# Kernel optimization log

Measured on AMD Instinct MI355X. Metric: run time of the kernel, lower is better.

Reference implementation:

```python
import jax, jax.numpy as jnp
import numpy as np


def setup_inputs() -> dict:
    key = jax.random.key(0)
    k1, k2 = jax.random.split(key)
    b, n, d = 4, 4096, 1024
    x = jax.random.normal(k1, (b, n, d), dtype=jnp.float32)
    t = jax.random.normal(k2, (2 * n, d), dtype=jnp.float32)
    return {"x": x, "t": t}


def reference(x, t):
    # x: (b, n, d); t: (2*l, d) with l = max(n, m); m = n here.
    n = x.shape[1]
    m = n
    l = max(n, m)
    L = 2 * l
    x_fft = jnp.fft.rfft(x, n=L, axis=-2)            # (b, L//2+1, d) complex
    t_fft = jnp.fft.rfft(t[None, :, :], n=L, axis=-2)  # (1, L//2+1, d)
    o = jnp.fft.irfft(x_fft * t_fft, n=L, axis=-2)   # (b, L, d)
    return o[:, :m]
```

## Files before the change

### kernel.cpp

```cpp
#include <hip/hip_runtime.h>
#include <hip/hip_bf16.h>

#define NFFT 8192
#define NH   4096
#define D    1024
#define NSEQ 4096
#define NDP  512
#define BATCH 4
#define NT   512
#define TSLOT 4097
#define PI_D 3.14159265358979323846

#define C1 0.92387953251128675613f
#define S1 0.38268343236508977173f
#define RT 0.70710678118654752440f

__device__ __forceinline__ int SWZ(int i) { return i ^ ((i >> 4) & 15) ^ ((i >> 8) & 15); }

__device__ __forceinline__ float2 cadd(float2 a, float2 b){ return make_float2(a.x+b.x, a.y+b.y); }
__device__ __forceinline__ float2 csub(float2 a, float2 b){ return make_float2(a.x-b.x, a.y-b.y); }
__device__ __forceinline__ float2 cmul(float2 a, float2 w){ return make_float2(a.x*w.x - a.y*w.y, a.x*w.y + a.y*w.x); }
__device__ __forceinline__ float2 cmulc(float2 a, float2 w){ return make_float2(a.x*w.x + a.y*w.y, a.y*w.x - a.x*w.y); }

__device__ __forceinline__ int drev16(int k) {
    return ((k & 1) << 12) | (((k >> 1) & 15) << 8) | (((k >> 5) & 15) << 4) | ((k >> 9) & 15);
}
__device__ __forceinline__ int kmap16(int tid, int it) {
    return ((tid >> 7) & 3) | (it << 2) | ((tid & 15) << 5) | (((tid >> 4) & 7) << 9);
}

__global__ __launch_bounds__(256) void wtab_init(float2* __restrict__ wtab) {
    int m = blockIdx.x * 256 + threadIdx.x;
    double a = -2.0 * PI_D * (double)m / (double)NFFT;
    wtab[m] = make_float2((float)cos(a), (float)sin(a));
}

template<int H, bool TW, bool INV>
__device__ __forceinline__ void pass16(float2* zs, const float2* __restrict__ wt, int t) {
    int blk = t >> 8;
    int i0, tw1i;
    if (H == 256)      { int j = t & 255;                      i0 = blk*4096 + j;           tw1i = 2*j;  }
    else if (H == 16)  { int g = (t>>4) & 15; int j = t & 15;  i0 = blk*4096 + g*256 + j;   tw1i = 32*j; }
    else               { int g = t & 255;                      i0 = blk*4096 + g*16;        tw1i = 0;    }

    float2 w1, w2, w3, w4, w8, w12;
    if (TW) {
        w1 = wt[tw1i];
        w2 = cmul(w1, w1);  w3 = cmul(w2, w1);
        w4 = cmul(w2, w2);  w8 = cmul(w4, w4);  w12 = cmul(w8, w4);
    }

    float2 v[16];
    #pragma unroll
    for (int q = 0; q < 16; ++q) v[q] = zs[SWZ(i0 + H*q)];

    if (INV && TW) {
        v[1]=cmulc(v[1],w1);  v[2]=cmulc(v[2],w2);  v[3]=cmulc(v[3],w3);
        v[4]=cmulc(v[4],w4);  v[5]=cmulc(v[5],cmul(w4,w1));  v[6]=cmulc(v[6],cmul(w4,w2));  v[7]=cmulc(v[7],cmul(w4,w3));
        v[8]=cmulc(v[8],w8);  v[9]=cmulc(v[9],cmul(w8,w1));  v[10]=cmulc(v[10],cmul(w8,w2)); v[11]=cmulc(v[11],cmul(w8,w3));
        v[12]=cmulc(v[12],w12); v[13]=cmulc(v[13],cmul(w12,w1)); v[14]=cmulc(v[14],cmul(w12,w2)); v[15]=cmulc(v[15],cmul(w12,w3));
    }

    float2 s[4][4];
    #pragma unroll
    for (int i = 0; i < 4; ++i) {
        float2 z0=v[i], z1=v[i+4], z2=v[i+8], z3=v[i+12];
        float2 A=cadd(z0,z2), Cc=csub(z0,z2), B=cadd(z1,z3), Dd=csub(z1,z3);
        s[i][0] = cadd(A,B);
        s[i][2] = csub(A,B);
        if (!INV) { s[i][1] = make_float2(Cc.x+Dd.y, Cc.y-Dd.x);
                    s[i][3] = make_float2(Cc.x-Dd.y, Cc.y+Dd.x); }
        else      { s[i][1] = make_float2(Cc.x-Dd.y, Cc.y+Dd.x);
                    s[i][3] = make_float2(Cc.x+Dd.y, Cc.y-Dd.x); }
    }
    if (!INV) {
        s[1][1]=cmul(s[1][1],make_float2(C1,-S1)); s[1][2]=cmul(s[1][2],make_float2(RT,-RT)); s[1][3]=cmul(s[1][3],make_float2(S1,-C1));
        s[2][1]=cmul(s[2][1],make_float2(RT,-RT)); s[2][2]=make_float2(s[2][2].y,-s[2][2].x); s[2][3]=cmul(s[2][3],make_float2(-RT,-RT));
        s[3][1]=cmul(s[3][1],make_float2(S1,-C1)); s[3][2]=cmul(s[3][2],make_float2(-RT,-RT)); s[3][3]=cmul(s[3][3],make_float2(-C1,S1));
    } else {
        s[1][1]=cmul(s[1][1],make_float2(C1,S1));  s[1][2]=cmul(s[1][2],make_float2(RT,RT));  s[1][3]=cmul(s[1][3],make_float2(S1,C1));
        s[2][1]=cmul(s[2][1],make_float2(RT,RT));  s[2][2]=make_float2(-s[2][2].y,s[2][2].x); s[2][3]=cmul(s[2][3],make_float2(-RT,RT));
        s[3][1]=cmul(s[3][1],make_float2(S1,C1));  s[3][2]=cmul(s[3][2],make_float2(-RT,RT)); s[3][3]=cmul(s[3][3],make_float2(-C1,-S1));
    }
    float2 y[16];
    #pragma unroll
    for (int o = 0; o < 4; ++o) {
        float2 z0=s[0][o], z1=s[1][o], z2=s[2][o], z3=s[3][o];
        float2 A=cadd(z0,z2), Cc=csub(z0,z2), B=cadd(z1,z3), Dd=csub(z1,z3);
        y[o]    = cadd(A,B);
        y[o+8]  = csub(A,B);
        if (!INV) { y[o+4]  = make_float2(Cc.x+Dd.y, Cc.y-Dd.x);
                    y[o+12] = make_float2(Cc.x-Dd.y, Cc.y+Dd.x); }
        else      { y[o+4]  = make_float2(Cc.x-Dd.y, Cc.y+Dd.x);
                    y[o+12] = make_float2(Cc.x+Dd.y, Cc.y-Dd.x); }
    }

    if (!INV && TW) {
        y[1]=cmul(y[1],w1);  y[2]=cmul(y[2],w2);  y[3]=cmul(y[3],w3);
        y[4]=cmul(y[4],w4);  y[5]=cmul(y[5],cmul(w4,w1));  y[6]=cmul(y[6],cmul(w4,w2));  y[7]=cmul(y[7],cmul(w4,w3));
        y[8]=cmul(y[8],w8);  y[9]=cmul(y[9],cmul(w8,w1));  y[10]=cmul(y[10],cmul(w8,w2)); y[11]=cmul(y[11],cmul(w8,w3));
        y[12]=cmul(y[12],w12); y[13]=cmul(y[13],cmul(w12,w1)); y[14]=cmul(y[14],cmul(w12,w2)); y[15]=cmul(y[15],cmul(w12,w3));
    }
    #pragma unroll
    for (int r = 0; r < 16; ++r) zs[SWZ(i0 + H*r)] = y[r];
}

template<int PACKED>
__global__ __launch_bounds__(NT, 2) void tspec_kernel(const float2* __restrict__ tP,
                                                      const float* __restrict__ tg,
                                                      const float2* __restrict__ wt,
                                                      float4* __restrict__ tspecU) {
    __shared__ float2 zs[NFFT];
    int t  = threadIdx.x;
    int dp = blockIdx.x;

    if (PACKED) {
        const float2* slab = tP + (size_t)dp * NFFT;
        #pragma unroll
        for (int it = 0; it < 8; ++it) {
            int idx = t + it * NT;
            float2 v0 = slab[idx], v1 = slab[idx + NH];
            zs[SWZ(idx)]      = cadd(v0, v1);
            zs[SWZ(idx + NH)] = cmul(csub(v0, v1), wt[idx]);
        }
    } else {
        const float* tb = tg + 2 * dp;
        #pragma unroll
        for (int it = 0; it < 8; ++it) {
            int idx = t + it * NT;
            float2 v0 = *(const float2*)(tb + (size_t)idx * D);
            float2 v1 = *(const float2*)(tb + (size_t)(idx + NH) * D);
            zs[SWZ(idx)]      = cadd(v0, v1);
            zs[SWZ(idx + NH)] = cmul(csub(v0, v1), wt[idx]);
        }
    }
    __syncthreads();
    pass16<256, true,  false>(zs, wt, t); __syncthreads();
    pass16<16,  true,  false>(zs, wt, t); __syncthreads();
    pass16<1,   false, false>(zs, wt, t); __syncthreads();

    float4* o = tspecU + (size_t)dp * TSLOT;
    #pragma unroll
    for (int it = 0; it < 8; ++it) {
        int k  = kmap16(t, it);
        int p1 = drev16(k);
        int p2 = drev16((NFFT - k) & (NFFT - 1));
        float2 z1 = zs[SWZ(p1)], z2 = zs[SWZ(p2)];
        o[it * NT + t] = make_float4(0.5f*(z1.x + z2.x), 0.5f*(z1.y - z2.y),
                                     0.5f*(z1.y + z2.y), 0.5f*(z2.x - z1.x));
    }
    if (t == 0) {
        float2 zn = zs[SWZ(8)];
        o[4096] = make_float4(zn.x, 0.f, zn.y, 0.f);
    }
}

template<int PACKED>
__global__ __launch_bounds__(NT, 2) void conv_kernel(float2* __restrict__ xP,
                                                     const float* __restrict__ xg,
                                                     float* __restrict__ outg,
                                                     const float2* __restrict__ wt,
                                                     const float4* __restrict__ tspecU) {
    __shared__ float2 zs[NFFT];
    int t  = threadIdx.x;
    int dp = blockIdx.x;
    int b  = blockIdx.y;

    float2* slab = PACKED ? (xP + ((size_t)dp * BATCH + b) * NSEQ) : nullptr;
    if (PACKED) {
        #pragma unroll
        for (int it = 0; it < 8; ++it) {
            int idx = t + it * NT;
            float2 v = slab[idx];
            zs[SWZ(idx)]      = v;
            zs[SWZ(idx + NH)] = cmul(v, wt[idx]);
        }
    } else {
        const float* xb = xg + (size_t)b * NSEQ * D + 2 * dp;
        #pragma unroll
        for (int it = 0; it < 8; ++it) {
            int idx = t + it * NT;
            float2 v = *(const float2*)(xb + (size_t)idx * D);
            zs[SWZ(idx)]      = v;
            zs[SWZ(idx + NH)] = cmul(v, wt[idx]);
        }
    }
    __syncthreads();
    pass16<256, true,  false>(zs, wt, t); __syncthreads();
    pass16<16,  true,  false>(zs, wt, t); __syncthreads();
    pass16<1,   false, false>(zs, wt, t); __syncthreads();

    const float4* ts4 = tspecU + (size_t)dp * TSLOT;
    #pragma unroll
    for (int it = 0; it < 8; ++it) {
        int k  = kmap16(t, it);
        int p1 = drev16(k);
        int p2 = drev16((NFFT - k) & (NFFT - 1));
        float2 z1 = zs[SWZ(p1)], z2 = zs[SWZ(p2)];
        float4 T  = ts4[it * NT + t];
        float x0r = 0.5f*(z1.x + z2.x), x0i = 0.5f*(z1.y - z2.y);
        float x1r = 0.5f*(z1.y + z2.y), x1i = 0.5f*(z2.x - z1.x);
        float y0r = x0r*T.x - x0i*T.y, y0i = x0r*T.y + x0i*T.x;
        float y1r = x1r*T.z - x1i*T.w, y1i = x1r*T.w + x1i*T.z;
        zs[SWZ(p1)] = make_float2(y0r - y1i, y0i + y1r);
        zs[SWZ(p2)] = make_float2(y0r + y1i, y1r - y0i);
    }
    if (t == 0) {
        float4 T = ts4[4096];
        float2 zn = zs[SWZ(8)];
        zs[SWZ(8)] = make_float2(zn.x * T.x, zn.y * T.z);
    }
    __syncthreads();

    pass16<1,   false, true>(zs, wt, t); __syncthreads();
    pass16<16,  true,  true>(zs, wt, t); __syncthreads();
    pass16<256, true,  true>(zs, wt, t); __syncthreads();

    const float sc = 1.0f / (float)NFFT;
    if (PACKED) {
        #pragma unroll
        for (int it = 0; it < 8; ++it) {
            int n = t + it * NT;
            float2 a  = zs[SWZ(n)];
            float2 bb = zs[SWZ(n + NH)];
            float2 r  = cadd(a, cmulc(bb, wt[n]));
            slab[n] = make_float2(r.x * sc, r.y * sc);
        }
    } else {
        float* ob = outg + (size_t)b * NSEQ * D + 2 * dp;
        #pragma unroll
        for (int it = 0; it < 8; ++it) {
            int n = t + it * NT;
            float2 a  = zs[SWZ(n)];
            float2 bb = zs[SWZ(n + NH)];
            float2 r  = cadd(a, cmulc(bb, wt[n]));
            *(float2*)(ob + (size_t)n * D) = make_float2(r.x * sc, r.y * sc);
        }
    }
}

__global__ __launch_bounds__(256) void pack_kernel(const float* __restrict__ in,
                                                   float2* __restrict__ outp,
                                                   int Nrows, int Bsz) {
    __shared__ float tile[64][65];
    int tid = threadIdx.x;
    int n0 = blockIdx.x * 64;
    int d0 = blockIdx.y * 64;
    int b  = blockIdx.z;
    const float* ib = in + (size_t)b * Nrows * D;
    #pragma unroll
    for (int it = 0; it < 16; ++it) {
        int n_l = it * 4 + (tid >> 6);
        int d_l = tid & 63;
        tile[n_l][d_l] = ib[(size_t)(n0 + n_l) * D + d0 + d_l];
    }
    __syncthreads();
    #pragma unroll
    for (int it = 0; it < 8; ++it) {
        int flat = it * 256 + tid;
        int dp_l = flat >> 6;
        int n_l  = flat & 63;
        float2 v = make_float2(tile[n_l][2*dp_l], tile[n_l][2*dp_l + 1]);
        outp[((size_t)(d0/2 + dp_l) * Bsz + b) * (size_t)Nrows + n0 + n_l] = v;
    }
}

__global__ __launch_bounds__(256) void unpack_kernel(const float2* __restrict__ in,
                                                     float* __restrict__ outp) {
    __shared__ float tile[64][65];
    int tid = threadIdx.x;
    int n0 = blockIdx.x * 64;
    int d0 = blockIdx.y * 64;
    int b  = blockIdx.z;
    #pragma unroll
    for (int it = 0; it < 8; ++it) {
        int flat = it * 256 + tid;
        int dp_l = flat >> 6;
        int n_l  = flat & 63;
        float2 v = in[((size_t)(d0/2 + dp_l) * BATCH + b) * (size_t)NSEQ + n0 + n_l];
        tile[n_l][2*dp_l]     = v.x;
        tile[n_l][2*dp_l + 1] = v.y;
    }
    __syncthreads();
    float* ob = outp + (size_t)b * NSEQ * D;
    #pragma unroll
    for (int it = 0; it < 16; ++it) {
        int n_l = it * 4 + (tid >> 6);
        int d_l = tid & 63;
        ob[(size_t)(n0 + n_l) * D + d0 + d_l] = tile[n_l][d_l];
    }
}

extern "C" void kernel_launch(void* const* d_in, const int* in_sizes, int n_in,
                              void* d_out, int out_size, void* d_ws, size_t ws_size,
                              hipStream_t stream) {
    const float* x = (const float*)d_in[0];
    const float* t = (const float*)d_in[1];
    float* outp = (float*)d_out;

    char* ws = (char*)d_ws;
    float2* wtab   = (float2*)ws;
    float4* tspecU = (float4*)(ws + 65536);
    const size_t OFF_REGION = 65536 + (size_t)NDP * TSLOT * 16;
    float2* region = (float2*)(ws + OFF_REGION);
    const size_t need_full = OFF_REGION + (size_t)NDP * BATCH * NSEQ * sizeof(float2);

    wtab_init<<<16, 256, 0, stream>>>(wtab);

    if (ws_size >= need_full) {
        pack_kernel<<<dim3(128, 16, 1), 256, 0, stream>>>(t, region, NFFT, 1);
        tspec_kernel<1><<<NDP, NT, 0, stream>>>(region, nullptr, wtab, tspecU);
        pack_kernel<<<dim3(64, 16, BATCH), 256, 0, stream>>>(x, region, NSEQ, BATCH);
        conv_kernel<1><<<dim3(NDP, BATCH, 1), NT, 0, stream>>>(region, nullptr, nullptr, wtab, tspecU);
        unpack_kernel<<<dim3(64, 16, BATCH), 256, 0, stream>>>(region, outp);
    } else {
        tspec_kernel<0><<<NDP, NT, 0, stream>>>(nullptr, t, wtab, tspecU);
        conv_kernel<0><<<dim3(NDP, BATCH, 1), NT, 0, stream>>>(nullptr, x, outp, wtab, tspecU);
    }
}
```

Baseline: 188.0 us.

## Fuse first/last FFT passes with global load/store and spectrum pointwise in registers

The first radix-16 pass now runs directly on values loaded from global memory, and the last inverse pass feeds the output store, so the separate LDS staging round trips are gone. The final forward pass and the pointwise spectrum multiply plus the first inverse pass stay in registers. Each thread reads its conjugate-pair partner from a computed mirror chunk instead of bit-reversed scattered reads. This removes several shared-memory passes and barriers. In exchange it adds complex index logic and keeps more registers live, which may reduce occupancy.

```diff
diff --git a/kernel.cpp b/kernel.cpp
--- a/kernel.cpp
+++ b/kernel.cpp
@@ -22,45 +22,14 @@
 __device__ __forceinline__ float2 cmul(float2 a, float2 w){ return make_float2(a.x*w.x - a.y*w.y, a.x*w.y + a.y*w.x); }
 __device__ __forceinline__ float2 cmulc(float2 a, float2 w){ return make_float2(a.x*w.x + a.y*w.y, a.y*w.x - a.x*w.y); }
 
-__device__ __forceinline__ int drev16(int k) {
-    return ((k & 1) << 12) | (((k >> 1) & 15) << 8) | (((k >> 5) & 15) << 4) | ((k >> 9) & 15);
-}
-__device__ __forceinline__ int kmap16(int tid, int it) {
-    return ((tid >> 7) & 3) | (it << 2) | ((tid & 15) << 5) | (((tid >> 4) & 7) << 9);
-}
-
 __global__ __launch_bounds__(256) void wtab_init(float2* __restrict__ wtab) {
     int m = blockIdx.x * 256 + threadIdx.x;
     double a = -2.0 * PI_D * (double)m / (double)NFFT;
     wtab[m] = make_float2((float)cos(a), (float)sin(a));
 }
 
-template<int H, bool TW, bool INV>
-__device__ __forceinline__ void pass16(float2* zs, const float2* __restrict__ wt, int t) {
-    int blk = t >> 8;
-    int i0, tw1i;
-    if (H == 256)      { int j = t & 255;                      i0 = blk*4096 + j;           tw1i = 2*j;  }
-    else if (H == 16)  { int g = (t>>4) & 15; int j = t & 15;  i0 = blk*4096 + g*256 + j;   tw1i = 32*j; }
-    else               { int g = t & 255;                      i0 = blk*4096 + g*16;        tw1i = 0;    }
-
-    float2 w1, w2, w3, w4, w8, w12;
-    if (TW) {
-        w1 = wt[tw1i];
-        w2 = cmul(w1, w1);  w3 = cmul(w2, w1);
-        w4 = cmul(w2, w2);  w8 = cmul(w4, w4);  w12 = cmul(w8, w4);
-    }
-
-    float2 v[16];
-    #pragma unroll
-    for (int q = 0; q < 16; ++q) v[q] = zs[SWZ(i0 + H*q)];
-
-    if (INV && TW) {
-        v[1]=cmulc(v[1],w1);  v[2]=cmulc(v[2],w2);  v[3]=cmulc(v[3],w3);
-        v[4]=cmulc(v[4],w4);  v[5]=cmulc(v[5],cmul(w4,w1));  v[6]=cmulc(v[6],cmul(w4,w2));  v[7]=cmulc(v[7],cmul(w4,w3));
-        v[8]=cmulc(v[8],w8);  v[9]=cmulc(v[9],cmul(w8,w1));  v[10]=cmulc(v[10],cmul(w8,w2)); v[11]=cmulc(v[11],cmul(w8,w3));
-        v[12]=cmulc(v[12],w12); v[13]=cmulc(v[13],cmul(w12,w1)); v[14]=cmulc(v[14],cmul(w12,w2)); v[15]=cmulc(v[15],cmul(w12,w3));
-    }
-
+template<bool INV>
+__device__ __forceinline__ void dft16(float2 v[16]) {
     float2 s[4][4];
     #pragma unroll
     for (int i = 0; i < 4; ++i) {
@@ -82,27 +51,65 @@
         s[2][1]=cmul(s[2][1],make_float2(RT,RT));  s[2][2]=make_float2(-s[2][2].y,s[2][2].x); s[2][3]=cmul(s[2][3],make_float2(-RT,RT));
         s[3][1]=cmul(s[3][1],make_float2(S1,C1));  s[3][2]=cmul(s[3][2],make_float2(-RT,RT)); s[3][3]=cmul(s[3][3],make_float2(-C1,-S1));
     }
-    float2 y[16];
     #pragma unroll
     for (int o = 0; o < 4; ++o) {
         float2 z0=s[0][o], z1=s[1][o], z2=s[2][o], z3=s[3][o];
         float2 A=cadd(z0,z2), Cc=csub(z0,z2), B=cadd(z1,z3), Dd=csub(z1,z3);
-        y[o]    = cadd(A,B);
-        y[o+8]  = csub(A,B);
-        if (!INV) { y[o+4]  = make_float2(Cc.x+Dd.y, Cc.y-Dd.x);
-                    y[o+12] = make_float2(Cc.x-Dd.y, Cc.y+Dd.x); }
-        else      { y[o+4]  = make_float2(Cc.x-Dd.y, Cc.y+Dd.x);
-                    y[o+12] = make_float2(Cc.x+Dd.y, Cc.y-Dd.x); }
-    }
-
-    if (!INV && TW) {
-        y[1]=cmul(y[1],w1);  y[2]=cmul(y[2],w2);  y[3]=cmul(y[3],w3);
-        y[4]=cmul(y[4],w4);  y[5]=cmul(y[5],cmul(w4,w1));  y[6]=cmul(y[6],cmul(w4,w2));  y[7]=cmul(y[7],cmul(w4,w3));
-        y[8]=cmul(y[8],w8);  y[9]=cmul(y[9],cmul(w8,w1));  y[10]=cmul(y[10],cmul(w8,w2)); y[11]=cmul(y[11],cmul(w8,w3));
-        y[12]=cmul(y[12],w12); y[13]=cmul(y[13],cmul(w12,w1)); y[14]=cmul(y[14],cmul(w12,w2)); y[15]=cmul(y[15],cmul(w12,w3));
-    }
-    #pragma unroll
-    for (int r = 0; r < 16; ++r) zs[SWZ(i0 + H*r)] = y[r];
+        v[o]    = cadd(A,B);
+        v[o+8]  = csub(A,B);
+        if (!INV) { v[o+4]  = make_float2(Cc.x+Dd.y, Cc.y-Dd.x);
+                    v[o+12] = make_float2(Cc.x-Dd.y, Cc.y+Dd.x); }
+        else      { v[o+4]  = make_float2(Cc.x-Dd.y, Cc.y+Dd.x);
+                    v[o+12] = make_float2(Cc.x+Dd.y, Cc.y-Dd.x); }
+    }
+}
+
+__device__ __forceinline__ void twiddle_fwd(float2 v[16], const float2* __restrict__ wt, int tw1i) {
+    float2 w1 = wt[tw1i];
+    float2 w2 = cmul(w1,w1), w3 = cmul(w2,w1), w4 = cmul(w2,w2), w8 = cmul(w4,w4), w12 = cmul(w8,w4);
+    v[1]=cmul(v[1],w1);  v[2]=cmul(v[2],w2);  v[3]=cmul(v[3],w3);
+    v[4]=cmul(v[4],w4);  v[5]=cmul(v[5],cmul(w4,w1));  v[6]=cmul(v[6],cmul(w4,w2));  v[7]=cmul(v[7],cmul(w4,w3));
+    v[8]=cmul(v[8],w8);  v[9]=cmul(v[9],cmul(w8,w1));  v[10]=cmul(v[10],cmul(w8,w2)); v[11]=cmul(v[11],cmul(w8,w3));
+    v[12]=cmul(v[12],w12); v[13]=cmul(v[13],cmul(w12,w1)); v[14]=cmul(v[14],cmul(w12,w2)); v[15]=cmul(v[15],cmul(w12,w3));
+}
+__device__ __forceinline__ void twiddle_inv(float2 v[16], const float2* __restrict__ wt, int tw1i) {
+    float2 w1 = wt[tw1i];
+    float2 w2 = cmul(w1,w1), w3 = cmul(w2,w1), w4 = cmul(w2,w2), w8 = cmul(w4,w4), w12 = cmul(w8,w4);
+    v[1]=cmulc(v[1],w1);  v[2]=cmulc(v[2],w2);  v[3]=cmulc(v[3],w3);
+    v[4]=cmulc(v[4],w4);  v[5]=cmulc(v[5],cmul(w4,w1));  v[6]=cmulc(v[6],cmul(w4,w2));  v[7]=cmulc(v[7],cmul(w4,w3));
+    v[8]=cmulc(v[8],w8);  v[9]=cmulc(v[9],cmul(w8,w1));  v[10]=cmulc(v[10],cmul(w8,w2)); v[11]=cmulc(v[11],cmul(w8,w3));
+    v[12]=cmulc(v[12],w12); v[13]=cmulc(v[13],cmul(w12,w1)); v[14]=cmulc(v[14],cmul(w12,w2)); v[15]=cmulc(v[15],cmul(w12,w3));
+}
+
+template<bool INV>
+__device__ __forceinline__ void pass16mid(float2* zs, const float2* __restrict__ wt, int t) {
+    int blk = t >> 8;
+    int g = (t >> 4) & 15, j = t & 15;
+    int i0 = blk*4096 + g*256 + j;
+    int tw1i = 32*j;
+    float2 v[16];
+    #pragma unroll
+    for (int q = 0; q < 16; ++q) v[q] = zs[SWZ(i0 + 16*q)];
+    if (INV) twiddle_inv(v, wt, tw1i);
+    dft16<INV>(v);
+    if (!INV) twiddle_fwd(v, wt, tw1i);
+    #pragma unroll
+    for (int r = 0; r < 16; ++r) zs[SWZ(i0 + 16*r)] = v[r];
+}
+
+__device__ __forceinline__ void pair_chunk(int b0, int d1, int d2,
+                                           int& pbase, int& br2, int& kbase) {
+    int nd1, nd2;
+    if (b0 == 0) {
+        int br1 = (d1 != 0);
+        nd1 = (16 - d1) & 15;
+        nd2 = (16 - d2 - br1) & 15;
+        br2 = ((d2 != 0) || br1) ? 1 : 0;
+    } else {
+        nd1 = 15 - d1; nd2 = 15 - d2; br2 = 1;
+    }
+    pbase = (((b0 << 8) | (nd1 << 4) | nd2) << 4);
+    kbase = b0 + 2*d1 + 32*d2;
 }
 
 template<int PACKED>
@@ -111,47 +118,50 @@
                                                       const float2* __restrict__ wt,
                                                       float4* __restrict__ tspecU) {
     __shared__ float2 zs[NFFT];
-    int t  = threadIdx.x;
-    int dp = blockIdx.x;
-
-    if (PACKED) {
-        const float2* slab = tP + (size_t)dp * NFFT;
-        #pragma unroll
-        for (int it = 0; it < 8; ++it) {
-            int idx = t + it * NT;
-            float2 v0 = slab[idx], v1 = slab[idx + NH];
-            zs[SWZ(idx)]      = cadd(v0, v1);
-            zs[SWZ(idx + NH)] = cmul(csub(v0, v1), wt[idx]);
+    int t = threadIdx.x, dp = blockIdx.x;
+    int blk = t >> 8, j = t & 255;
+    float2 v[16];
+
+    #pragma unroll
+    for (int q = 0; q < 16; ++q) {
+        int n = j + (q << 8);
+        float2 a, c;
+        if (PACKED) { const float2* s_ = tP + (size_t)dp * NFFT; a = s_[n]; c = s_[n + NH]; }
+        else { const float* tb = tg + 2*dp; a = *(const float2*)(tb + (size_t)n*D); c = *(const float2*)(tb + (size_t)(n+NH)*D); }
+        v[q] = blk ? cmul(csub(a, c), wt[n]) : cadd(a, c);
+    }
+    dft16<false>(v);
+    twiddle_fwd(v, wt, 2*j);
+    #pragma unroll
+    for (int r = 0; r < 16; ++r) zs[SWZ((blk<<12) + j + (r<<8))] = v[r];
+    __syncthreads();
+
+    pass16mid<false>(zs, wt, t);
+    __syncthreads();
+
+    int b0 = blk, d1 = t & 15, d2 = (t >> 4) & 15;
+    int i0 = (((b0 << 8) | (d1 << 4) | d2) << 4);
+    #pragma unroll
+    for (int q = 0; q < 16; ++q) v[q] = zs[SWZ(i0 + q)];
+    dft16<false>(v);
+    #pragma unroll
+    for (int q = 0; q < 16; ++q) zs[SWZ(i0 + q)] = v[q];
+    __syncthreads();
+
+    int pbase, br2, kbase;
+    pair_chunk(b0, d1, d2, pbase, br2, kbase);
+    float4* o = tspecU + (size_t)dp * TSLOT;
+    #pragma unroll
+    for (int q = 0; q < 16; ++q) {
+        int k = kbase + (q << 9);
+        bool lo = (q < 8) || (k <= 4096);
+        if (lo) {
+            int qp = (16 - q - br2) & 15;
+            float2 z1 = v[q];
+            float2 z2 = zs[SWZ(pbase + qp)];
+            o[k] = make_float4(0.5f*(z1.x + z2.x), 0.5f*(z1.y - z2.y),
+                               0.5f*(z1.y + z2.y), 0.5f*(z2.x - z1.x));
         }
-    } else {
-        const float* tb = tg + 2 * dp;
-        #pragma unroll
-        for (int it = 0; it < 8; ++it) {
-            int idx = t + it * NT;
-            float2 v0 = *(const float2*)(tb + (size_t)idx * D);
-            float2 v1 = *(const float2*)(tb + (size_t)(idx + NH) * D);
-            zs[SWZ(idx)]      = cadd(v0, v1);
-            zs[SWZ(idx + NH)] = cmul(csub(v0, v1), wt[idx]);
-        }
-    }
-    __syncthreads();
-    pass16<256, true,  false>(zs, wt, t); __syncthreads();
-    pass16<16,  true,  false>(zs, wt, t); __syncthreads();
-    pass16<1,   false, false>(zs, wt, t); __syncthreads();
-
-    float4* o = tspecU + (size_t)dp * TSLOT;
-    #pragma unroll
-    for (int it = 0; it < 8; ++it) {
-        int k  = kmap16(t, it);
-        int p1 = drev16(k);
-        int p2 = drev16((NFFT - k) & (NFFT - 1));
-        float2 z1 = zs[SWZ(p1)], z2 = zs[SWZ(p2)];
-        o[it * NT + t] = make_float4(0.5f*(z1.x + z2.x), 0.5f*(z1.y - z2.y),
-                                     0.5f*(z1.y + z2.y), 0.5f*(z2.x - z1.x));
-    }
-    if (t == 0) {
-        float2 zn = zs[SWZ(8)];
-        o[4096] = make_float4(zn.x, 0.f, zn.y, 0.f);
     }
 }
 
@@ -162,79 +172,90 @@
                                                      const float2* __restrict__ wt,
                                                      const float4* __restrict__ tspecU) {
     __shared__ float2 zs[NFFT];
-    int t  = threadIdx.x;
-    int dp = blockIdx.x;
-    int b  = blockIdx.y;
-
+    int t = threadIdx.x;
+    int dp = blockIdx.x, b = blockIdx.y;
+    int blk = t >> 8, j = t & 255;
+    float2 v[16];
     float2* slab = PACKED ? (xP + ((size_t)dp * BATCH + b) * NSEQ) : nullptr;
-    if (PACKED) {
-        #pragma unroll
-        for (int it = 0; it < 8; ++it) {
-            int idx = t + it * NT;
-            float2 v = slab[idx];
-            zs[SWZ(idx)]      = v;
-            zs[SWZ(idx + NH)] = cmul(v, wt[idx]);
-        }
-    } else {
-        const float* xb = xg + (size_t)b * NSEQ * D + 2 * dp;
-        #pragma unroll
-        for (int it = 0; it < 8; ++it) {
-            int idx = t + it * NT;
-            float2 v = *(const float2*)(xb + (size_t)idx * D);
-            zs[SWZ(idx)]      = v;
-            zs[SWZ(idx + NH)] = cmul(v, wt[idx]);
-        }
-    }
-    __syncthreads();
-    pass16<256, true,  false>(zs, wt, t); __syncthreads();
-    pass16<16,  true,  false>(zs, wt, t); __syncthreads();
-    pass16<1,   false, false>(zs, wt, t); __syncthreads();
+    const float* xb = PACKED ? nullptr : (xg + (size_t)b * NSEQ * D + 2 * dp);
+
+    #pragma unroll
+    for (int q = 0; q < 16; ++q) {
+        int n = j + (q << 8);
+        float2 xv = PACKED ? slab[n] : *(const float2*)(xb + (size_t)n * D);
+        v[q] = blk ? cmul(xv, wt[n]) : xv;
+    }
+    dft16<false>(v);
+    twiddle_fwd(v, wt, 2*j);
+    #pragma unroll
+    for (int r = 0; r < 16; ++r) zs[SWZ((blk<<12) + j + (r<<8))] = v[r];
+    __syncthreads();
+
+    pass16mid<false>(zs, wt, t);
+    __syncthreads();
+
+    int b0 = blk, d1 = t & 15, d2 = (t >> 4) & 15;
+    int i0 = (((b0 << 8) | (d1 << 4) | d2) << 4);
+    #pragma unroll
+    for (int q = 0; q < 16; ++q) v[q] = zs[SWZ(i0 + q)];
+    dft16<false>(v);
+    #pragma unroll
+    for (int q = 0; q < 16; ++q) zs[SWZ(i0 + q)] = v[q];
+    __syncthreads();
+
+    int pbase, br2, kbase;
+    pair_chunk(b0, d1, d2, pbase, br2, kbase);
+    float2 u[16];
+    #pragma unroll
+    for (int q = 0; q < 16; ++q) {
+        int qp = (16 - q - br2) & 15;
+        u[q] = zs[SWZ(pbase + qp)];
+    }
+    __syncthreads();
 
     const float4* ts4 = tspecU + (size_t)dp * TSLOT;
     #pragma unroll
-    for (int it = 0; it < 8; ++it) {
-        int k  = kmap16(t, it);
-        int p1 = drev16(k);
-        int p2 = drev16((NFFT - k) & (NFFT - 1));
-        float2 z1 = zs[SWZ(p1)], z2 = zs[SWZ(p2)];
-        float4 T  = ts4[it * NT + t];
+    for (int q = 0; q < 16; ++q) {
+        int k = kbase + (q << 9);
+        bool lo = (q < 8) || (k <= 4096);
+        int kr = lo ? k : 8192 - k;
+        float2 z1 = lo ? v[q] : u[q];
+        float2 z2 = lo ? u[q] : v[q];
+        float4 T = ts4[kr];
         float x0r = 0.5f*(z1.x + z2.x), x0i = 0.5f*(z1.y - z2.y);
         float x1r = 0.5f*(z1.y + z2.y), x1i = 0.5f*(z2.x - z1.x);
         float y0r = x0r*T.x - x0i*T.y, y0i = x0r*T.y + x0i*T.x;
         float y1r = x1r*T.z - x1i*T.w, y1i = x1r*T.w + x1i*T.z;
-        zs[SWZ(p1)] = make_float2(y0r - y1i, y0i + y1r);
-        zs[SWZ(p2)] = make_float2(y0r + y1i, y1r - y0i);
-    }
-    if (t == 0) {
-        float4 T = ts4[4096];
-        float2 zn = zs[SWZ(8)];
-        zs[SWZ(8)] = make_float2(zn.x * T.x, zn.y * T.z);
-    }
-    __syncthreads();
-
-    pass16<1,   false, true>(zs, wt, t); __syncthreads();
-    pass16<16,  true,  true>(zs, wt, t); __syncthreads();
-    pass16<256, true,  true>(zs, wt, t); __syncthreads();
-
-    const float sc = 1.0f / (float)NFFT;
-    if (PACKED) {
+        v[q] = lo ? make_float2(y0r - y1i, y0i + y1r)
+                  : make_float2(y0r + y1i, y1r - y0i);
+    }
+    dft16<true>(v);
+    #pragma unroll
+    for (int q = 0; q < 16; ++q) zs[SWZ(i0 + q)] = v[q];
+    __syncthreads();
+
+    pass16mid<true>(zs, wt, t);
+    __syncthreads();
+
+    #pragma unroll
+    for (int q = 0; q < 16; ++q) v[q] = zs[SWZ((blk<<12) + j + (q<<8))];
+    twiddle_inv(v, wt, 2*j);
+    dft16<true>(v);
+    if (blk == 1) {
         #pragma unroll
-        for (int it = 0; it < 8; ++it) {
-            int n = t + it * NT;
-            float2 a  = zs[SWZ(n)];
-            float2 bb = zs[SWZ(n + NH)];
-            float2 r  = cadd(a, cmulc(bb, wt[n]));
-            slab[n] = make_float2(r.x * sc, r.y * sc);
-        }
-    } else {
-        float* ob = outg + (size_t)b * NSEQ * D + 2 * dp;
+        for (int q = 0; q < 16; ++q) zs[SWZ((1<<12) + j + (q<<8))] = v[q];
+    }
+    __syncthreads();
+    if (blk == 0) {
+        const float sc = 1.0f / (float)NFFT;
         #pragma unroll
-        for (int it = 0; it < 8; ++it) {
-            int n = t + it * NT;
-            float2 a  = zs[SWZ(n)];
-            float2 bb = zs[SWZ(n + NH)];
-            float2 r  = cadd(a, cmulc(bb, wt[n]));
-            *(float2*)(ob + (size_t)n * D) = make_float2(r.x * sc, r.y * sc);
+        for (int q = 0; q < 16; ++q) {
+            int n = j + (q << 8);
+            float2 bb = zs[SWZ((1<<12) + n)];
+            float2 r = cadd(v[q], cmulc(bb, wt[n]));
+            r = make_float2(r.x * sc, r.y * sc);
+            if (PACKED) slab[n] = r;
+            else *(float2*)(outg + (size_t)b * NSEQ * D + (size_t)n * D + 2 * dp) = r;
         }
     }
 }
```

Result: slower. 208.2 us (+10.8%).

## Drop pack/unpack transposes and remap blocks so each XCD gets contiguous channels

Applied to the files above, without the earlier changes.

Removes the separate pack and unpack transpose kernels and their workspace round trip. The FFT kernels now read x and t directly with strided 8-byte loads and write the output directly. To keep those strided accesses cache friendly, the 1D grid is remapped so blocks that land on the same XCD (round-robin by block index mod 8) handle adjacent channel pairs and can share cache lines in that XCD's L2. This saves two full-tensor transposes plus extra launches, at the cost of poorly coalesced direct accesses that depend on L2 reuse across neighbouring blocks.

```diff
diff --git a/kernel.cpp b/kernel.cpp
--- a/kernel.cpp
+++ b/kernel.cpp
@@ -105,34 +105,22 @@
     for (int r = 0; r < 16; ++r) zs[SWZ(i0 + H*r)] = y[r];
 }
 
-template<int PACKED>
-__global__ __launch_bounds__(NT, 2) void tspec_kernel(const float2* __restrict__ tP,
-                                                      const float* __restrict__ tg,
+__global__ __launch_bounds__(NT, 2) void tspec_kernel(const float* __restrict__ tg,
                                                       const float2* __restrict__ wt,
                                                       float4* __restrict__ tspecU) {
     __shared__ float2 zs[NFFT];
+    int wg = blockIdx.x;
+    int dp = ((wg & 7) << 6) | (wg >> 3);
     int t  = threadIdx.x;
-    int dp = blockIdx.x;
-
-    if (PACKED) {
-        const float2* slab = tP + (size_t)dp * NFFT;
-        #pragma unroll
-        for (int it = 0; it < 8; ++it) {
-            int idx = t + it * NT;
-            float2 v0 = slab[idx], v1 = slab[idx + NH];
-            zs[SWZ(idx)]      = cadd(v0, v1);
-            zs[SWZ(idx + NH)] = cmul(csub(v0, v1), wt[idx]);
-        }
-    } else {
-        const float* tb = tg + 2 * dp;
-        #pragma unroll
-        for (int it = 0; it < 8; ++it) {
-            int idx = t + it * NT;
-            float2 v0 = *(const float2*)(tb + (size_t)idx * D);
-            float2 v1 = *(const float2*)(tb + (size_t)(idx + NH) * D);
-            zs[SWZ(idx)]      = cadd(v0, v1);
-            zs[SWZ(idx + NH)] = cmul(csub(v0, v1), wt[idx]);
-        }
+
+    const float* tb = tg + 2 * dp;
+    #pragma unroll
+    for (int it = 0; it < 8; ++it) {
+        int idx = t + it * NT;
+        float2 v0 = *(const float2*)(tb + (size_t)idx * D);
+        float2 v1 = *(const float2*)(tb + (size_t)(idx + NH) * D);
+        zs[SWZ(idx)]      = cadd(v0, v1);
+        zs[SWZ(idx + NH)] = cmul(csub(v0, v1), wt[idx]);
     }
     __syncthreads();
     pass16<256, true,  false>(zs, wt, t); __syncthreads();
@@ -155,35 +143,24 @@
     }
 }
 
-template<int PACKED>
-__global__ __launch_bounds__(NT, 2) void conv_kernel(float2* __restrict__ xP,
-                                                     const float* __restrict__ xg,
+__global__ __launch_bounds__(NT, 2) void conv_kernel(const float* __restrict__ xg,
                                                      float* __restrict__ outg,
                                                      const float2* __restrict__ wt,
                                                      const float4* __restrict__ tspecU) {
     __shared__ float2 zs[NFFT];
+    int wg = blockIdx.x;
+    int xcd = wg & 7, ix = wg >> 3;
+    int b  = ix >> 6;
+    int dp = (xcd << 6) | (ix & 63);
     int t  = threadIdx.x;
-    int dp = blockIdx.x;
-    int b  = blockIdx.y;
-
-    float2* slab = PACKED ? (xP + ((size_t)dp * BATCH + b) * NSEQ) : nullptr;
-    if (PACKED) {
-        #pragma unroll
-        for (int it = 0; it < 8; ++it) {
-            int idx = t + it * NT;
-            float2 v = slab[idx];
-            zs[SWZ(idx)]      = v;
-            zs[SWZ(idx + NH)] = cmul(v, wt[idx]);
-        }
-    } else {
-        const float* xb = xg + (size_t)b * NSEQ * D + 2 * dp;
-        #pragma unroll
-        for (int it = 0; it < 8; ++it) {
-            int idx = t + it * NT;
-            float2 v = *(const float2*)(xb + (size_t)idx * D);
-            zs[SWZ(idx)]      = v;
-            zs[SWZ(idx + NH)] = cmul(v, wt[idx]);
-        }
+
+    const float* xb = xg + (size_t)b * NSEQ * D + 2 * dp;
+    #pragma unroll
+    for (int it = 0; it < 8; ++it) {
+        int idx = t + it * NT;
+        float2 v = *(const float2*)(xb + (size_t)idx * D);
+        zs[SWZ(idx)]      = v;
+        zs[SWZ(idx + NH)] = cmul(v, wt[idx]);
     }
     __syncthreads();
     pass16<256, true,  false>(zs, wt, t); __syncthreads();
@@ -217,77 +194,14 @@
     pass16<256, true,  true>(zs, wt, t); __syncthreads();
 
     const float sc = 1.0f / (float)NFFT;
-    if (PACKED) {
-        #pragma unroll
-        for (int it = 0; it < 8; ++it) {
-            int n = t + it * NT;
-            float2 a  = zs[SWZ(n)];
-            float2 bb = zs[SWZ(n + NH)];
-            float2 r  = cadd(a, cmulc(bb, wt[n]));
-            slab[n] = make_float2(r.x * sc, r.y * sc);
-        }
-    } else {
-        float* ob = outg + (size_t)b * NSEQ * D + 2 * dp;
-        #pragma unroll
-        for (int it = 0; it < 8; ++it) {
-            int n = t + it * NT;
-            float2 a  = zs[SWZ(n)];
-            float2 bb = zs[SWZ(n + NH)];
-            float2 r  = cadd(a, cmulc(bb, wt[n]));
-            *(float2*)(ob + (size_t)n * D) = make_float2(r.x * sc, r.y * sc);
-        }
-    }
-}
-
-__global__ __launch_bounds__(256) void pack_kernel(const float* __restrict__ in,
-                                                   float2* __restrict__ outp,
-                                                   int Nrows, int Bsz) {
-    __shared__ float tile[64][65];
-    int tid = threadIdx.x;
-    int n0 = blockIdx.x * 64;
-    int d0 = blockIdx.y * 64;
-    int b  = blockIdx.z;
-    const float* ib = in + (size_t)b * Nrows * D;
-    #pragma unroll
-    for (int it = 0; it < 16; ++it) {
-        int n_l = it * 4 + (tid >> 6);
-        int d_l = tid & 63;
-        tile[n_l][d_l] = ib[(size_t)(n0 + n_l) * D + d0 + d_l];
-    }
-    __syncthreads();
-    #pragma unroll
-    for (int it = 0; it < 8; ++it) {
-        int flat = it * 256 + tid;
-        int dp_l = flat >> 6;
-        int n_l  = flat & 63;
-        float2 v = make_float2(tile[n_l][2*dp_l], tile[n_l][2*dp_l + 1]);
-        outp[((size_t)(d0/2 + dp_l) * Bsz + b) * (size_t)Nrows + n0 + n_l] = v;
-    }
-}
-
-__global__ __launch_bounds__(256) void unpack_kernel(const float2* __restrict__ in,
-                                                     float* __restrict__ outp) {
-    __shared__ float tile[64][65];
-    int tid = threadIdx.x;
-    int n0 = blockIdx.x * 64;
-    int d0 = blockIdx.y * 64;
-    int b  = blockIdx.z;
-    #pragma unroll
-    for (int it = 0; it < 8; ++it) {
-        int flat = it * 256 + tid;
-        int dp_l = flat >> 6;
-        int n_l  = flat & 63;
-        float2 v = in[((size_t)(d0/2 + dp_l) * BATCH + b) * (size_t)NSEQ + n0 + n_l];
-        tile[n_l][2*dp_l]     = v.x;
-        tile[n_l][2*dp_l + 1] = v.y;
-    }
-    __syncthreads();
-    float* ob = outp + (size_t)b * NSEQ * D;
-    #pragma unroll
-    for (int it = 0; it < 16; ++it) {
-        int n_l = it * 4 + (tid >> 6);
-        int d_l = tid & 63;
-        ob[(size_t)(n0 + n_l) * D + d0 + d_l] = tile[n_l][d_l];
+    float* ob = outg + (size_t)b * NSEQ * D + 2 * dp;
+    #pragma unroll
+    for (int it = 0; it < 8; ++it) {
+        int n = t + it * NT;
+        float2 a  = zs[SWZ(n)];
+        float2 bb = zs[SWZ(n + NH)];
+        float2 r  = cadd(a, cmulc(bb, wt[n]));
+        *(float2*)(ob + (size_t)n * D) = make_float2(r.x * sc, r.y * sc);
     }
 }
 
@@ -301,20 +215,8 @@
     char* ws = (char*)d_ws;
     float2* wtab   = (float2*)ws;
     float4* tspecU = (float4*)(ws + 65536);
-    const size_t OFF_REGION = 65536 + (size_t)NDP * TSLOT * 16;
-    float2* region = (float2*)(ws + OFF_REGION);
-    const size_t need_full = OFF_REGION + (size_t)NDP * BATCH * NSEQ * sizeof(float2);
 
     wtab_init<<<16, 256, 0, stream>>>(wtab);
-
-    if (ws_size >= need_full) {
-        pack_kernel<<<dim3(128, 16, 1), 256, 0, stream>>>(t, region, NFFT, 1);
-        tspec_kernel<1><<<NDP, NT, 0, stream>>>(region, nullptr, wtab, tspecU);
-        pack_kernel<<<dim3(64, 16, BATCH), 256, 0, stream>>>(x, region, NSEQ, BATCH);
-        conv_kernel<1><<<dim3(NDP, BATCH, 1), NT, 0, stream>>>(region, nullptr, nullptr, wtab, tspecU);
-        unpack_kernel<<<dim3(64, 16, BATCH), 256, 0, stream>>>(region, outp);
-    } else {
-        tspec_kernel<0><<<NDP, NT, 0, stream>>>(nullptr, t, wtab, tspecU);
-        conv_kernel<0><<<dim3(NDP, BATCH, 1), NT, 0, stream>>>(nullptr, x, outp, wtab, tspecU);
-    }
-}
+    tspec_kernel<<<NDP, NT, 0, stream>>>(t, wtab, tspecU);
+    conv_kernel<<<NDP * BATCH, NT, 0, stream>>>(x, outp, wtab, tspecU);
+}
```

New measurement: 193.5 us. 2.9% more time.

## Drop t packing, remap blocks across XCDs, prefetch spectrum into registers

Applied to the files above, without the earlier changes.

Removes the pack pass over t. tspec_kernel now reads t directly with strided accesses, and blocks are remapped so that neighbouring column pairs land on the same XCD, which should improve L2 sharing of the strided rows. The conv kernels load the precomputed t spectrum into registers before the forward FFT, so that global load latency overlaps with compute. A separate strided conv kernel with XCD-aware block mapping is added for the fallback path. The trade-offs are more register pressure and uncoalesced strided reads of t in the default path.

```diff
diff --git a/kernel.cpp b/kernel.cpp
--- a/kernel.cpp
+++ b/kernel.cpp
@@ -105,34 +105,22 @@
     for (int r = 0; r < 16; ++r) zs[SWZ(i0 + H*r)] = y[r];
 }
 
-template<int PACKED>
-__global__ __launch_bounds__(NT, 2) void tspec_kernel(const float2* __restrict__ tP,
-                                                      const float* __restrict__ tg,
+__global__ __launch_bounds__(NT, 2) void tspec_kernel(const float* __restrict__ tg,
                                                       const float2* __restrict__ wt,
                                                       float4* __restrict__ tspecU) {
     __shared__ float2 zs[NFFT];
+    int wg = blockIdx.x;
+    int dp = ((wg & 7) << 6) | (wg >> 3);
     int t  = threadIdx.x;
-    int dp = blockIdx.x;
-
-    if (PACKED) {
-        const float2* slab = tP + (size_t)dp * NFFT;
-        #pragma unroll
-        for (int it = 0; it < 8; ++it) {
-            int idx = t + it * NT;
-            float2 v0 = slab[idx], v1 = slab[idx + NH];
-            zs[SWZ(idx)]      = cadd(v0, v1);
-            zs[SWZ(idx + NH)] = cmul(csub(v0, v1), wt[idx]);
-        }
-    } else {
-        const float* tb = tg + 2 * dp;
-        #pragma unroll
-        for (int it = 0; it < 8; ++it) {
-            int idx = t + it * NT;
-            float2 v0 = *(const float2*)(tb + (size_t)idx * D);
-            float2 v1 = *(const float2*)(tb + (size_t)(idx + NH) * D);
-            zs[SWZ(idx)]      = cadd(v0, v1);
-            zs[SWZ(idx + NH)] = cmul(csub(v0, v1), wt[idx]);
-        }
+
+    const float* tb = tg + 2 * dp;
+    #pragma unroll
+    for (int it = 0; it < 8; ++it) {
+        int idx = t + it * NT;
+        float2 v0 = *(const float2*)(tb + (size_t)idx * D);
+        float2 v1 = *(const float2*)(tb + (size_t)(idx + NH) * D);
+        zs[SWZ(idx)]      = cadd(v0, v1);
+        zs[SWZ(idx + NH)] = cmul(csub(v0, v1), wt[idx]);
     }
     __syncthreads();
     pass16<256, true,  false>(zs, wt, t); __syncthreads();
@@ -155,49 +143,39 @@
     }
 }
 
-template<int PACKED>
-__global__ __launch_bounds__(NT, 2) void conv_kernel(float2* __restrict__ xP,
-                                                     const float* __restrict__ xg,
-                                                     float* __restrict__ outg,
-                                                     const float2* __restrict__ wt,
-                                                     const float4* __restrict__ tspecU) {
+__global__ __launch_bounds__(NT, 2) void conv_kernel_p(float2* __restrict__ xP,
+                                                       const float2* __restrict__ wt,
+                                                       const float4* __restrict__ tspecU) {
     __shared__ float2 zs[NFFT];
     int t  = threadIdx.x;
     int dp = blockIdx.x;
     int b  = blockIdx.y;
 
-    float2* slab = PACKED ? (xP + ((size_t)dp * BATCH + b) * NSEQ) : nullptr;
-    if (PACKED) {
-        #pragma unroll
-        for (int it = 0; it < 8; ++it) {
-            int idx = t + it * NT;
-            float2 v = slab[idx];
-            zs[SWZ(idx)]      = v;
-            zs[SWZ(idx + NH)] = cmul(v, wt[idx]);
-        }
-    } else {
-        const float* xb = xg + (size_t)b * NSEQ * D + 2 * dp;
-        #pragma unroll
-        for (int it = 0; it < 8; ++it) {
-            int idx = t + it * NT;
-            float2 v = *(const float2*)(xb + (size_t)idx * D);
-            zs[SWZ(idx)]      = v;
-            zs[SWZ(idx + NH)] = cmul(v, wt[idx]);
-        }
+    const float4* ts4 = tspecU + (size_t)dp * TSLOT;
+    float4 Tp[8];
+    #pragma unroll
+    for (int it = 0; it < 8; ++it) Tp[it] = ts4[it * NT + t];
+
+    float2* slab = xP + ((size_t)dp * BATCH + b) * NSEQ;
+    #pragma unroll
+    for (int it = 0; it < 8; ++it) {
+        int idx = t + it * NT;
+        float2 v = slab[idx];
+        zs[SWZ(idx)]      = v;
+        zs[SWZ(idx + NH)] = cmul(v, wt[idx]);
     }
     __syncthreads();
     pass16<256, true,  false>(zs, wt, t); __syncthreads();
     pass16<16,  true,  false>(zs, wt, t); __syncthreads();
     pass16<1,   false, false>(zs, wt, t); __syncthreads();
 
-    const float4* ts4 = tspecU + (size_t)dp * TSLOT;
     #pragma unroll
     for (int it = 0; it < 8; ++it) {
         int k  = kmap16(t, it);
         int p1 = drev16(k);
         int p2 = drev16((NFFT - k) & (NFFT - 1));
         float2 z1 = zs[SWZ(p1)], z2 = zs[SWZ(p2)];
-        float4 T  = ts4[it * NT + t];
+        float4 T  = Tp[it];
         float x0r = 0.5f*(z1.x + z2.x), x0i = 0.5f*(z1.y - z2.y);
         float x1r = 0.5f*(z1.y + z2.y), x1i = 0.5f*(z2.x - z1.x);
         float y0r = x0r*T.x - x0i*T.y, y0i = x0r*T.y + x0i*T.x;
@@ -217,25 +195,79 @@
     pass16<256, true,  true>(zs, wt, t); __syncthreads();
 
     const float sc = 1.0f / (float)NFFT;
-    if (PACKED) {
-        #pragma unroll
-        for (int it = 0; it < 8; ++it) {
-            int n = t + it * NT;
-            float2 a  = zs[SWZ(n)];
-            float2 bb = zs[SWZ(n + NH)];
-            float2 r  = cadd(a, cmulc(bb, wt[n]));
-            slab[n] = make_float2(r.x * sc, r.y * sc);
-        }
-    } else {
-        float* ob = outg + (size_t)b * NSEQ * D + 2 * dp;
-        #pragma unroll
-        for (int it = 0; it < 8; ++it) {
-            int n = t + it * NT;
-            float2 a  = zs[SWZ(n)];
-            float2 bb = zs[SWZ(n + NH)];
-            float2 r  = cadd(a, cmulc(bb, wt[n]));
-            *(float2*)(ob + (size_t)n * D) = make_float2(r.x * sc, r.y * sc);
-        }
+    #pragma unroll
+    for (int it = 0; it < 8; ++it) {
+        int n = t + it * NT;
+        float2 a  = zs[SWZ(n)];
+        float2 bb = zs[SWZ(n + NH)];
+        float2 r  = cadd(a, cmulc(bb, wt[n]));
+        slab[n] = make_float2(r.x * sc, r.y * sc);
+    }
+}
+
+__global__ __launch_bounds__(NT, 2) void conv_kernel_s(const float* __restrict__ xg,
+                                                       float* __restrict__ outg,
+                                                       const float2* __restrict__ wt,
+                                                       const float4* __restrict__ tspecU) {
+    __shared__ float2 zs[NFFT];
+    int wg = blockIdx.x;
+    int xcd = wg & 7, ix = wg >> 3;
+    int b  = ix >> 6;
+    int dp = (xcd << 6) | (ix & 63);
+    int t  = threadIdx.x;
+
+    const float4* ts4 = tspecU + (size_t)dp * TSLOT;
+    float4 Tp[8];
+    #pragma unroll
+    for (int it = 0; it < 8; ++it) Tp[it] = ts4[it * NT + t];
+
+    const float* xb = xg + (size_t)b * NSEQ * D + 2 * dp;
+    #pragma unroll
+    for (int it = 0; it < 8; ++it) {
+        int idx = t + it * NT;
+        float2 v = *(const float2*)(xb + (size_t)idx * D);
+        zs[SWZ(idx)]      = v;
+        zs[SWZ(idx + NH)] = cmul(v, wt[idx]);
+    }
+    __syncthreads();
+    pass16<256, true,  false>(zs, wt, t); __syncthreads();
+    pass16<16,  true,  false>(zs, wt, t); __syncthreads();
+    pass16<1,   false, false>(zs, wt, t); __syncthreads();
+
+    #pragma unroll
+    for (int it = 0; it < 8; ++it) {
+        int k  = kmap16(t, it);
+        int p1 = drev16(k);
+        int p2 = drev16((NFFT - k) & (NFFT - 1));
+        float2 z1 = zs[SWZ(p1)], z2 = zs[SWZ(p2)];
+        float4 T  = Tp[it];
+        float x0r = 0.5f*(z1.x + z2.x), x0i = 0.5f*(z1.y - z2.y);
+        float x1r = 0.5f*(z1.y + z2.y), x1i = 0.5f*(z2.x - z1.x);
+        float y0r = x0r*T.x - x0i*T.y, y0i = x0r*T.y + x0i*T.x;
+        float y1r = x1r*T.z - x1i*T.w, y1i = x1r*T.w + x1i*T.z;
+        zs[SWZ(p1)] = make_float2(y0r - y1i, y0i + y1r);
+        zs[SWZ(p2)] = make_float2(y0r + y1i, y1r - y0i);
+    }
+    if (t == 0) {
+        float4 T = ts4[4096];
+        float2 zn = zs[SWZ(8)];
+        zs[SWZ(8)] = make_float2(zn.x * T.x, zn.y * T.z);
+    }
+    __syncthreads();
+
+    pass16<1,   false, true>(zs, wt, t); __syncthreads();
+    pass16<16,  true,  true>(zs, wt, t); __syncthreads();
+    pass16<256, true,  true>(zs, wt, t); __syncthreads();
+
+    const float sc = 1.0f / (float)NFFT;
+    float* ob = outg + (size_t)b * NSEQ * D + 2 * dp;
+    #pragma unroll
+    for (int it = 0; it < 8; ++it) {
+        int n = t + it * NT;
+        float2 a  = zs[SWZ(n)];
+        float2 bb = zs[SWZ(n + NH)];
+        float2 r  = cadd(a, cmulc(bb, wt[n]));
+        *(float2*)(ob + (size_t)n * D) = make_float2(r.x * sc, r.y * sc);
     }
 }
 
@@ -301,20 +333,19 @@
     char* ws = (char*)d_ws;
     float2* wtab   = (float2*)ws;
     float4* tspecU = (float4*)(ws + 65536);
-    const size_t OFF_REGION = 65536 + (size_t)NDP * TSLOT * 16;
-    float2* region = (float2*)(ws + OFF_REGION);
-    const size_t need_full = OFF_REGION + (size_t)NDP * BATCH * NSEQ * sizeof(float2);
+    const size_t OFF_XP = 65536 + (size_t)NDP * TSLOT * 16;
+    float2* xP = (float2*)(ws + OFF_XP);
+    const size_t need_full = OFF_XP + (size_t)NDP * BATCH * NSEQ * sizeof(float2);
 
     wtab_init<<<16, 256, 0, stream>>>(wtab);
 
     if (ws_size >= need_full) {
-        pack_kernel<<<dim3(128, 16, 1), 256, 0, stream>>>(t, region, NFFT, 1);
-        tspec_kernel<1><<<NDP, NT, 0, stream>>>(region, nullptr, wtab, tspecU);
-        pack_kernel<<<dim3(64, 16, BATCH), 256, 0, stream>>>(x, region, NSEQ, BATCH);
-        conv_kernel<1><<<dim3(NDP, BATCH, 1), NT, 0, stream>>>(region, nullptr, nullptr, wtab, tspecU);
-        unpack_kernel<<<dim3(64, 16, BATCH), 256, 0, stream>>>(region, outp);
+        tspec_kernel<<<NDP, NT, 0, stream>>>(t, wtab, tspecU);
+        pack_kernel<<<dim3(64, 16, BATCH), 256, 0, stream>>>(x, xP, NSEQ, BATCH);
+        conv_kernel_p<<<dim3(NDP, BATCH, 1), NT, 0, stream>>>(xP, wtab, tspecU);
+        unpack_kernel<<<dim3(64, 16, BATCH), 256, 0, stream>>>(xP, outp);
     } else {
-        tspec_kernel<0><<<NDP, NT, 0, stream>>>(nullptr, t, wtab, tspecU);
-        conv_kernel<0><<<dim3(NDP, BATCH, 1), NT, 0, stream>>>(nullptr, x, outp, wtab, tspecU);
-    }
-}
+        tspec_kernel<<<NDP, NT, 0, stream>>>(t, wtab, tspecU);
+        conv_kernel_s<<<NDP * BATCH, NT, 0, stream>>>(x, outp, wtab, tspecU);
+    }
+}
```

Result: slower. 195.5 us (+4.0%).
